# Kernel optimization log

Hardware: AMD Instinct MI355X
Metric: run time of the kernel (lower is better)

The kernel has to match this reference:

```python
import jax, jax.numpy as jnp
import numpy as np

D_MODEL = 1024
NHEADS = 16
DIM_K = D_MODEL // NHEADS


def setup_inputs() -> dict:
    key = jax.random.key(0)
    ks = jax.random.split(key, 7)
    B, S = 4, 2048
    scale = 1.0 / np.sqrt(D_MODEL)
    return {
        "Q": jax.random.normal(ks[0], (B, S, D_MODEL), jnp.float32),
        "K": jax.random.normal(ks[1], (B, S, D_MODEL), jnp.float32),
        "V": jax.random.normal(ks[2], (B, S, D_MODEL), jnp.float32),
        "Wq": jax.random.normal(ks[3], (D_MODEL, D_MODEL), jnp.float32) * scale,
        "Wk": jax.random.normal(ks[4], (D_MODEL, D_MODEL), jnp.float32) * scale,
        "Wv": jax.random.normal(ks[5], (D_MODEL, D_MODEL), jnp.float32) * scale,
        "Wo": jax.random.normal(ks[6], (D_MODEL, D_MODEL), jnp.float32) * scale,
    }


def _split(x):
    # [B,S,D] -> [B,H,S,dk]
    B, S, _ = x.shape
    return x.reshape(B, S, NHEADS, DIM_K).transpose(0, 2, 1, 3)


def reference(Q, K, V, Wq, Wk, Wv, Wo):
    # nn.Linear(x) = x @ W.T; weights stored torch-style [out, in]
    q = _split(Q @ Wq.T)  # [B,H,S,dk]
    k = _split(K @ Wk.T)
    v = _split(V @ Wv.T)
    scores = jnp.einsum("bhsd,bhtd->bhst", q, k) / jnp.sqrt(jnp.float32(DIM_K))
    attn = jax.nn.softmax(scores, axis=-1)
    out = jnp.einsum("bhst,bhtd->bhsd", attn, v)  # [B,H,S,dk]
    B, H, S, dk = out.shape
    out = out.transpose(0, 2, 1, 3).reshape(B, S, H * dk)
    return out @ Wo.T
```

## Files before the change

kernel.cpp:

```cpp
#include <hip/hip_runtime.h>
#include <math.h>
#include <stdint.h>

#define D_MODEL 1024
#define NHEADS  16
#define DK      64
#define BATCH   4
#define SEQ     2048
#define MROWS   (BATCH * SEQ)
#define TENS    ((size_t)MROWS * D_MODEL)
#define WELT    ((size_t)D_MODEL * D_MODEL)

typedef __attribute__((ext_vector_type(8))) _Float16 f16x8;
typedef __attribute__((ext_vector_type(2))) __fp16 h16x2;
typedef __attribute__((ext_vector_type(4))) float f32x4;
typedef __attribute__((ext_vector_type(8))) unsigned short us8;
typedef __attribute__((ext_vector_type(4))) unsigned short us4;

__device__ __forceinline__ unsigned short f2h(float x) {
    _Float16 h = (_Float16)x;
    return __builtin_bit_cast(unsigned short, h);
}

#if __has_builtin(__builtin_amdgcn_exp2f)
__device__ __forceinline__ float fexp2(float x) { return __builtin_amdgcn_exp2f(x); }
#else
__device__ __forceinline__ float fexp2(float x) { return exp2f(x); }
#endif

__device__ __forceinline__ void gld_lds16(const void* g, void* l) {
    __builtin_amdgcn_global_load_lds(
        (__attribute__((address_space(1))) void*)(uintptr_t)(g),
        (__attribute__((address_space(3))) void*)(unsigned)(uintptr_t)(l),
        16, 0, 0);
}

__global__ __launch_bounds__(256)
void convert_kernel(const float* __restrict__ q, const float* __restrict__ k,
                    const float* __restrict__ v, const float* __restrict__ wq,
                    const float* __restrict__ wk, const float* __restrict__ wv,
                    const float* __restrict__ wo, unsigned short* __restrict__ dst)
{
    const int seg = blockIdx.y;
    size_t i = ((size_t)blockIdx.x * 256 + threadIdx.x) * 4;
    const float* src;
    size_t doff, soff;
    if (seg < 3) {
        if (i >= TENS) return;
        src = (seg == 0) ? q : (seg == 1) ? k : v;
        soff = i;
        doff = (size_t)seg * TENS + i;
    } else {
        if (i >= 4 * WELT) return;
        const int widx = (int)(i >> 20);
        src = (widx == 0) ? wq : (widx == 1) ? wk : (widx == 2) ? wv : wo;
        soff = i & (WELT - 1);
        doff = 3 * TENS + i;
    }
    float4 f = *(const float4*)(src + soff);
    us4 o = { f2h(f.x), f2h(f.y), f2h(f.z), f2h(f.w) };
    *(us4*)(dst + doff) = o;
}

__device__ __forceinline__
void gemm_body8(const unsigned short* __restrict__ A,
                const unsigned short* __restrict__ B,
                void* __restrict__ C, int N, int K, int omode,
                unsigned short* As, unsigned short* Bs)
{
    const int tid  = threadIdx.x;
    const int wave = tid >> 6;
    const int lane = tid & 63;
    const int g    = lane >> 4;
    const int m15  = lane & 15;
    const int bm   = blockIdx.x * 256;
    const int bn   = blockIdx.y * 128;

    const int srw = lane >> 3;
    const int lc  = (lane & 7) ^ srw;

    const int wr = (wave >> 1) * 64;
    const int wc = (wave & 1) * 64;

    f32x4 acc[4][4];
#pragma unroll
    for (int i = 0; i < 4; ++i)
#pragma unroll
        for (int j = 0; j < 4; ++j) acc[i][j] = (f32x4){0.f, 0.f, 0.f, 0.f};

    auto stage = [&](int buf, int t) {
        const int k0 = t * 64;
#pragma unroll
        for (int i = 0; i < 4; ++i) {
            const int rb = i * 64 + wave * 8;
            gld_lds16(A + (size_t)(bm + rb + srw) * K + k0 + lc * 8,
                      &As[buf * (256 * 64) + rb * 64]);
        }
#pragma unroll
        for (int j = 0; j < 2; ++j) {
            const int rb = j * 64 + wave * 8;
            gld_lds16(B + (size_t)(bn + rb + srw) * K + k0 + lc * 8,
                      &Bs[buf * (128 * 64) + rb * 64]);
        }
    };

    auto compute = [&](int buf) {
        const unsigned short* Ab = &As[buf * (256 * 64)];
        const unsigned short* Bb = &Bs[buf * (128 * 64)];
#pragma unroll
        for (int t = 0; t < 2; ++t) {
            f16x8 af[4], bf[4];
#pragma unroll
            for (int i = 0; i < 4; ++i) {
                int row = wr + i * 16 + m15;
                int pc  = (4 * t + g) ^ (row & 7);
                af[i] = *(const f16x8*)&Ab[row * 64 + pc * 8];
            }
#pragma unroll
            for (int j = 0; j < 4; ++j) {
                int row = wc + j * 16 + m15;
                int pc  = (4 * t + g) ^ (row & 7);
                bf[j] = *(const f16x8*)&Bb[row * 64 + pc * 8];
            }
            __builtin_amdgcn_s_setprio(1);
#pragma unroll
            for (int i = 0; i < 4; ++i)
#pragma unroll
                for (int j = 0; j < 4; ++j)
                    acc[i][j] = __builtin_amdgcn_mfma_f32_16x16x32_f16(
                        af[i], bf[j], acc[i][j], 0, 0, 0);
            __builtin_amdgcn_s_setprio(0);
        }
    };

    const int NT = K / 64;
    stage(0, 0);
    stage(1, 1);
    int cur = 0;
    for (int t = 0; t < NT; ++t) {
        if (t + 2 < NT) {
            int nb = cur + 2; if (nb >= 3) nb -= 3;
            stage(nb, t + 2);
            asm volatile("s_waitcnt vmcnt(12)" ::: "memory");
        } else if (t + 1 < NT) {
            asm volatile("s_waitcnt vmcnt(6)" ::: "memory");
        } else {
            asm volatile("s_waitcnt vmcnt(0)" ::: "memory");
        }
        __builtin_amdgcn_s_barrier();
        __builtin_amdgcn_sched_barrier(0);
        compute(cur);
        __builtin_amdgcn_sched_barrier(0);
        __builtin_amdgcn_s_barrier();
        ++cur; if (cur == 3) cur = 0;
    }

#pragma unroll
    for (int i = 0; i < 4; ++i) {
        const int gm0 = bm + wr + i * 16 + g * 4;
#pragma unroll
        for (int j = 0; j < 4; ++j) {
            const int gn = bn + wc + j * 16 + m15;
            if (omode == 0) {
#pragma unroll
                for (int r = 0; r < 4; ++r)
                    ((float*)C)[(size_t)(gm0 + r) * N + gn] = acc[i][j][r];
            } else if (omode == 1) {
#pragma unroll
                for (int r = 0; r < 4; ++r)
                    ((unsigned short*)C)[(size_t)(gm0 + r) * N + gn] = f2h(acc[i][j][r]);
            } else {
                const int b_ = gm0 >> 11, s_ = gm0 & 2047;
                const int h_ = gn >> 6,  d_ = gn & 63;
                us4 o = { f2h(acc[i][j][0]), f2h(acc[i][j][1]),
                          f2h(acc[i][j][2]), f2h(acc[i][j][3]) };
                *(us4*)((unsigned short*)C +
                        (((size_t)(b_ * NHEADS + h_) * 256 + (s_ >> 3)) * 64 + d_) * 8
                        + (s_ & 7)) = o;
            }
        }
    }
}

__global__ __launch_bounds__(512)
void proj3_kernel(const unsigned short* __restrict__ qb,
                  const unsigned short* __restrict__ kb,
                  const unsigned short* __restrict__ vb,
                  const unsigned short* __restrict__ wq,
                  const unsigned short* __restrict__ wk,
                  const unsigned short* __restrict__ wv,
                  unsigned short* __restrict__ qproj,
                  unsigned short* __restrict__ kproj,
                  unsigned short* __restrict__ vtw)
{
    __shared__ unsigned short As[3 * 256 * 64];
    __shared__ unsigned short Bs[3 * 128 * 64];
    const int z = blockIdx.z;
    const unsigned short* A = (z == 0) ? qb : (z == 1) ? kb : vb;
    const unsigned short* B = (z == 0) ? wq : (z == 1) ? wk : wv;
    void* C = (z == 0) ? (void*)qproj : (z == 1) ? (void*)kproj : (void*)vtw;
    gemm_body8(A, B, C, D_MODEL, D_MODEL, (z == 2) ? 2 : 1, As, Bs);
}

__global__ __launch_bounds__(512)
void gemm_out_kernel(const unsigned short* __restrict__ A,
                     const unsigned short* __restrict__ B,
                     float* __restrict__ C)
{
    __shared__ unsigned short As[3 * 256 * 64];
    __shared__ unsigned short Bs[3 * 128 * 64];
    gemm_body8(A, B, C, D_MODEL, D_MODEL, 0, As, Bs);
}

__global__ __launch_bounds__(256, 2)
void attn_kernel(const unsigned short* __restrict__ qp,
                 const unsigned short* __restrict__ kp,
                 const unsigned short* __restrict__ vt,
                 unsigned short* __restrict__ ao)
{
    __shared__ unsigned short Ks[2][64 * 64];
    __shared__ unsigned short VTs[2][64 * 64];
    __shared__ unsigned short Ps[4][16 * 72];

    const int tid = threadIdx.x;
    const int w = tid >> 6, lane = tid & 63;
    const int g = lane >> 4, m15 = lane & 15;
    const int qt = blockIdx.x, h = blockIdx.y, b = blockIdx.z;

    const int q0 = qt * 256 + w * 64;
    const size_t rowbase = (size_t)b * SEQ;

    const int srw = lane >> 3;
    const int lc  = (lane & 7) ^ srw;

    const _Float16 qscale = (_Float16)(0.125f * 1.4426950408889634f);
    f16x8 qf[4][2];
#pragma unroll
    for (int mi = 0; mi < 4; ++mi)
#pragma unroll
        for (int t = 0; t < 2; ++t) {
            f16x8 v = *(const f16x8*)(qp + (rowbase + q0 + mi * 16 + m15) * D_MODEL
                                      + h * DK + t * 32 + g * 8);
            qf[mi][t] = v * qscale;
        }

    const _Float16 one16 = (_Float16)1.f;
    const f16x8 onesf = { one16, one16, one16, one16, one16, one16, one16, one16 };

    float mrun[4] = {-INFINITY, -INFINITY, -INFINITY, -INFINITY};
    float lrun[4] = {0.f, 0.f, 0.f, 0.f};

    f32x4 accO[4][4];
#pragma unroll
    for (int mi = 0; mi < 4; ++mi)
#pragma unroll
        for (int i = 0; i < 4; ++i) accO[mi][i] = (f32x4){0.f, 0.f, 0.f, 0.f};

    const unsigned short* kbase = kp + rowbase * D_MODEL + h * DK;
    const unsigned short* vbase = vt + (size_t)(b * NHEADS + h) * DK * SEQ;

    auto stage = [&](int buf, int t) {
#pragma unroll
        for (int it = 0; it < 2; ++it) {
            const int rb = w * 16 + it * 8;
            gld_lds16(kbase + (size_t)(t * 64 + rb + srw) * D_MODEL + lc * 8,
                      &Ks[buf][rb * 64]);
            gld_lds16(vbase + ((size_t)(t * 8 + lc) * 64 + rb + srw) * 8,
                      &VTs[buf][rb * 64]);
        }
    };

    const int NT = SEQ / 64;
    stage(0, 0);
    __syncthreads();

    for (int kt = 0; kt < NT; ++kt) {
        const int cur = kt & 1;
        if (kt + 1 < NT) stage(cur ^ 1, kt + 1);

        f32x4 ST[4][4];
        __builtin_amdgcn_s_setprio(1);
#pragma unroll
        for (int km = 0; km < 4; ++km) {
            const int row = km * 16 + m15;
            f16x8 kf0 = *(const f16x8*)&Ks[cur][row * 64 + ((0 + g) ^ (row & 7)) * 8];
            f16x8 kf1 = *(const f16x8*)&Ks[cur][row * 64 + ((4 + g) ^ (row & 7)) * 8];
#pragma unroll
            for (int mi = 0; mi < 4; ++mi) {
                f32x4 z = (f32x4){0.f, 0.f, 0.f, 0.f};
                z = __builtin_amdgcn_mfma_f32_16x16x32_f16(kf0, qf[mi][0], z, 0, 0, 0);
                z = __builtin_amdgcn_mfma_f32_16x16x32_f16(kf1, qf[mi][1], z, 0, 0, 0);
                ST[km][mi] = z;
            }
        }
        __builtin_amdgcn_s_setprio(0);

        float scl[4];
        f16x8 pf[4][2];
#pragma unroll
        for (int mi = 0; mi < 4; ++mi) {
            float t0 = fmaxf(fmaxf(ST[0][mi][0], ST[0][mi][1]), ST[0][mi][2]);
            float t1 = fmaxf(fmaxf(ST[0][mi][3], ST[1][mi][0]), ST[1][mi][1]);
            float t2 = fmaxf(fmaxf(ST[1][mi][2], ST[1][mi][3]), ST[2][mi][0]);
            float t3 = fmaxf(fmaxf(ST[2][mi][1], ST[2][mi][2]), ST[2][mi][3]);
            float t4 = fmaxf(fmaxf(ST[3][mi][0], ST[3][mi][1]), ST[3][mi][2]);
            float u0 = fmaxf(fmaxf(t0, t1), t2);
            float u1 = fmaxf(fmaxf(t3, t4), ST[3][mi][3]);
            float mx = fmaxf(u0, u1);
            mx = fmaxf(mx, __shfl_xor(mx, 16));
            mx = fmaxf(mx, __shfl_xor(mx, 32));
            float mnew = fmaxf(mrun[mi], mx);
            scl[mi] = fexp2(mrun[mi] - mnew);
            mrun[mi] = mnew;
#pragma unroll
            for (int km = 0; km < 4; ++km) {
                float p0 = fexp2(ST[km][mi][0] - mnew);
                float p1 = fexp2(ST[km][mi][1] - mnew);
                float p2 = fexp2(ST[km][mi][2] - mnew);
                float p3 = fexp2(ST[km][mi][3] - mnew);
                h16x2 d0 = __builtin_amdgcn_cvt_pkrtz(p0, p1);
                h16x2 d1 = __builtin_amdgcn_cvt_pkrtz(p2, p3);
                uint2 wv = { __builtin_bit_cast(unsigned, d0),
                             __builtin_bit_cast(unsigned, d1) };
                *(uint2*)&Ps[w][m15 * 72 + km * 16 + g * 4] = wv;
            }
            pf[mi][0] = *(const f16x8*)&Ps[w][m15 * 72 + g * 8];
            pf[mi][1] = *(const f16x8*)&Ps[w][m15 * 72 + 32 + g * 8];
            f32x4 zs = (f32x4){0.f, 0.f, 0.f, 0.f};
            zs = __builtin_amdgcn_mfma_f32_16x16x32_f16(onesf, pf[mi][0], zs, 0, 0, 0);
            zs = __builtin_amdgcn_mfma_f32_16x16x32_f16(onesf, pf[mi][1], zs, 0, 0, 0);
            lrun[mi] = lrun[mi] * scl[mi] + zs[0];
        }

        int chg = (scl[0] < 1.f) | (scl[1] < 1.f) | (scl[2] < 1.f) | (scl[3] < 1.f);
        if (__any(chg)) {
#pragma unroll
            for (int mi = 0; mi < 4; ++mi)
#pragma unroll
                for (int i = 0; i < 4; ++i) accO[mi][i] *= scl[mi];
        }

        __builtin_amdgcn_s_setprio(1);
#pragma unroll
        for (int i = 0; i < 4; ++i) {
            const int row = i * 16 + m15;
            f16x8 vf0 = *(const f16x8*)&VTs[cur][row * 64 + ((0 + g) ^ (row & 7)) * 8];
            f16x8 vf1 = *(const f16x8*)&VTs[cur][row * 64 + ((4 + g) ^ (row & 7)) * 8];
#pragma unroll
            for (int mi = 0; mi < 4; ++mi) {
                f32x4 a = accO[mi][i];
                a = __builtin_amdgcn_mfma_f32_16x16x32_f16(vf0, pf[mi][0], a, 0, 0, 0);
                a = __builtin_amdgcn_mfma_f32_16x16x32_f16(vf1, pf[mi][1], a, 0, 0, 0);
                accO[mi][i] = a;
            }
        }
        __builtin_amdgcn_s_setprio(0);

        __syncthreads();
    }

#pragma unroll
    for (int mi = 0; mi < 4; ++mi) {
        const float li = 1.f / lrun[mi];
        const size_t qg = rowbase + q0 + mi * 16 + m15;
#pragma unroll
        for (int i = 0; i < 4; ++i) {
            us4 o = { f2h(accO[mi][i][0] * li), f2h(accO[mi][i][1] * li),
                      f2h(accO[mi][i][2] * li), f2h(accO[mi][i][3] * li) };
            *(us4*)(ao + qg * D_MODEL + h * DK + i * 16 + g * 4) = o;
        }
    }
}

extern "C" void kernel_launch(void* const* d_in, const int* in_sizes, int n_in,
                              void* d_out, int out_size, void* d_ws, size_t ws_size,
                              hipStream_t stream)
{
    const float* Q  = (const float*)d_in[0];
    const float* K  = (const float*)d_in[1];
    const float* V  = (const float*)d_in[2];
    const float* Wq = (const float*)d_in[3];
    const float* Wk = (const float*)d_in[4];
    const float* Wv = (const float*)d_in[5];
    const float* Wo = (const float*)d_in[6];

    unsigned short* base = (unsigned short*)d_ws;
    unsigned short* qb = base;
    unsigned short* kb = qb + TENS;
    unsigned short* vb = kb + TENS;
    unsigned short* wq = vb + TENS;
    unsigned short* wk = wq + WELT;
    unsigned short* wv = wk + WELT;
    unsigned short* wo = wv + WELT;
    unsigned short* qproj = wo + WELT;
    unsigned short* kproj = qproj + TENS;
    unsigned short* vtw   = kproj + TENS;
    unsigned short* aow   = vtw + TENS;

    convert_kernel<<<dim3(TENS / 1024, 4), 256, 0, stream>>>(Q, K, V, Wq, Wk, Wv, Wo, base);

    proj3_kernel<<<dim3(MROWS / 256, D_MODEL / 128, 3), 512, 0, stream>>>(
        qb, kb, vb, wq, wk, wv, qproj, kproj, vtw);

    attn_kernel<<<dim3(SEQ / 256, NHEADS, BATCH), 256, 0, stream>>>(
        qproj, kproj, vtw, aow);

    gemm_out_kernel<<<dim3(MROWS / 256, D_MODEL / 128), 512, 0, stream>>>(
        aow, wo, (float*)d_out);
}
```

Baseline: 329.6 us.

## Shrink GEMM tiles to 128x128 with double buffering; keep attention P in registers

The projection and output GEMMs move from 256x128 tiles with 512 threads and triple-buffered LDS to 128x128 tiles with 256 threads, two LDS buffers and two blocks per CU. The next tile is now staged after the compute barrier. In attention, the softmax probabilities no longer round-trip through LDS. The code switches to 16x16x16 MFMAs whose B-operand layout matches the score accumulator registers, so P can feed the PV and row-sum MFMAs directly. This trades LDS traffic and a per-wave scratch buffer for twice as many MFMA issues, plus a shallower prefetch pipeline in the GEMMs.

New measurement: 343.3 us. 1.04x slower.

```diff
diff --git a/kernel.cpp b/kernel.cpp
--- a/kernel.cpp
+++ b/kernel.cpp
@@ -12,6 +12,7 @@
 #define WELT    ((size_t)D_MODEL * D_MODEL)
 
 typedef __attribute__((ext_vector_type(8))) _Float16 f16x8;
+typedef __attribute__((ext_vector_type(4))) _Float16 f16x4;
 typedef __attribute__((ext_vector_type(2))) __fp16 h16x2;
 typedef __attribute__((ext_vector_type(4))) float f32x4;
 typedef __attribute__((ext_vector_type(8))) unsigned short us8;
@@ -27,6 +28,15 @@
 #else
 __device__ __forceinline__ float fexp2(float x) { return exp2f(x); }
 #endif
+
+__device__ __forceinline__ f32x4 mfma16(f16x4 a, f16x4 b, f32x4 c) {
+#if __has_builtin(__builtin_amdgcn_mfma_f32_16x16x16f16)
+    return __builtin_amdgcn_mfma_f32_16x16x16f16(a, b, c, 0, 0, 0);
+#else
+    asm("v_mfma_f32_16x16x16_f16 %0, %1, %2, %0" : "+v"(c) : "v"(a), "v"(b));
+    return c;
+#endif
+}
 
 __device__ __forceinline__ void gld_lds16(const void* g, void* l) {
     __builtin_amdgcn_global_load_lds(
@@ -63,17 +73,17 @@
 }
 
 __device__ __forceinline__
-void gemm_body8(const unsigned short* __restrict__ A,
-                const unsigned short* __restrict__ B,
-                void* __restrict__ C, int N, int K, int omode,
-                unsigned short* As, unsigned short* Bs)
+void gemm_body(const unsigned short* __restrict__ A,
+               const unsigned short* __restrict__ B,
+               void* __restrict__ C, int N, int K, int omode,
+               unsigned short* As, unsigned short* Bs)
 {
     const int tid  = threadIdx.x;
     const int wave = tid >> 6;
     const int lane = tid & 63;
     const int g    = lane >> 4;
     const int m15  = lane & 15;
-    const int bm   = blockIdx.x * 256;
+    const int bm   = blockIdx.x * 128;
     const int bn   = blockIdx.y * 128;
 
     const int srw = lane >> 3;
@@ -92,20 +102,16 @@
         const int k0 = t * 64;
 #pragma unroll
         for (int i = 0; i < 4; ++i) {
-            const int rb = i * 64 + wave * 8;
+            const int rb = wave * 32 + i * 8;
             gld_lds16(A + (size_t)(bm + rb + srw) * K + k0 + lc * 8,
-                      &As[buf * (256 * 64) + rb * 64]);
-        }
-#pragma unroll
-        for (int j = 0; j < 2; ++j) {
-            const int rb = j * 64 + wave * 8;
+                      &As[buf * (128 * 64) + rb * 64]);
             gld_lds16(B + (size_t)(bn + rb + srw) * K + k0 + lc * 8,
                       &Bs[buf * (128 * 64) + rb * 64]);
         }
     };
 
     auto compute = [&](int buf) {
-        const unsigned short* Ab = &As[buf * (256 * 64)];
+        const unsigned short* Ab = &As[buf * (128 * 64)];
         const unsigned short* Bb = &Bs[buf * (128 * 64)];
 #pragma unroll
         for (int t = 0; t < 2; ++t) {
@@ -138,12 +144,8 @@
     stage(1, 1);
     int cur = 0;
     for (int t = 0; t < NT; ++t) {
-        if (t + 2 < NT) {
-            int nb = cur + 2; if (nb >= 3) nb -= 3;
-            stage(nb, t + 2);
-            asm volatile("s_waitcnt vmcnt(12)" ::: "memory");
-        } else if (t + 1 < NT) {
-            asm volatile("s_waitcnt vmcnt(6)" ::: "memory");
+        if (t + 1 < NT) {
+            asm volatile("s_waitcnt vmcnt(8)" ::: "memory");
         } else {
             asm volatile("s_waitcnt vmcnt(0)" ::: "memory");
         }
@@ -152,7 +154,8 @@
         compute(cur);
         __builtin_amdgcn_sched_barrier(0);
         __builtin_amdgcn_s_barrier();
-        ++cur; if (cur == 3) cur = 0;
+        if (t + 2 < NT) stage(cur, t + 2);
+        cur ^= 1;
     }
 
 #pragma unroll
@@ -182,7 +185,7 @@
     }
 }
 
-__global__ __launch_bounds__(512)
+__global__ __launch_bounds__(256, 2)
 void proj3_kernel(const unsigned short* __restrict__ qb,
                   const unsigned short* __restrict__ kb,
                   const unsigned short* __restrict__ vb,
@@ -193,23 +196,23 @@
                   unsigned short* __restrict__ kproj,
                   unsigned short* __restrict__ vtw)
 {
-    __shared__ unsigned short As[3 * 256 * 64];
-    __shared__ unsigned short Bs[3 * 128 * 64];
+    __shared__ unsigned short As[2 * 128 * 64];
+    __shared__ unsigned short Bs[2 * 128 * 64];
     const int z = blockIdx.z;
     const unsigned short* A = (z == 0) ? qb : (z == 1) ? kb : vb;
     const unsigned short* B = (z == 0) ? wq : (z == 1) ? wk : wv;
     void* C = (z == 0) ? (void*)qproj : (z == 1) ? (void*)kproj : (void*)vtw;
-    gemm_body8(A, B, C, D_MODEL, D_MODEL, (z == 2) ? 2 : 1, As, Bs);
-}
-
-__global__ __launch_bounds__(512)
+    gemm_body(A, B, C, D_MODEL, D_MODEL, (z == 2) ? 2 : 1, As, Bs);
+}
+
+__global__ __launch_bounds__(256, 2)
 void gemm_out_kernel(const unsigned short* __restrict__ A,
                      const unsigned short* __restrict__ B,
                      float* __restrict__ C)
 {
-    __shared__ unsigned short As[3 * 256 * 64];
-    __shared__ unsigned short Bs[3 * 128 * 64];
-    gemm_body8(A, B, C, D_MODEL, D_MODEL, 0, As, Bs);
+    __shared__ unsigned short As[2 * 128 * 64];
+    __shared__ unsigned short Bs[2 * 128 * 64];
+    gemm_body(A, B, C, D_MODEL, D_MODEL, 0, As, Bs);
 }
 
 __global__ __launch_bounds__(256, 2)
@@ -220,7 +223,6 @@
 {
     __shared__ unsigned short Ks[2][64 * 64];
     __shared__ unsigned short VTs[2][64 * 64];
-    __shared__ unsigned short Ps[4][16 * 72];
 
     const int tid = threadIdx.x;
     const int w = tid >> 6, lane = tid & 63;
@@ -245,7 +247,7 @@
         }
 
     const _Float16 one16 = (_Float16)1.f;
-    const f16x8 onesf = { one16, one16, one16, one16, one16, one16, one16, one16 };
+    const f16x4 ones4 = { one16, one16, one16, one16 };
 
     float mrun[4] = {-INFINITY, -INFINITY, -INFINITY, -INFINITY};
     float lrun[4] = {0.f, 0.f, 0.f, 0.f};
@@ -296,7 +298,7 @@
         __builtin_amdgcn_s_setprio(0);
 
         float scl[4];
-        f16x8 pf[4][2];
+        f16x4 pb[4][4];
 #pragma unroll
         for (int mi = 0; mi < 4; ++mi) {
             float t0 = fmaxf(fmaxf(ST[0][mi][0], ST[0][mi][1]), ST[0][mi][2]);
@@ -322,13 +324,11 @@
                 h16x2 d1 = __builtin_amdgcn_cvt_pkrtz(p2, p3);
                 uint2 wv = { __builtin_bit_cast(unsigned, d0),
                              __builtin_bit_cast(unsigned, d1) };
-                *(uint2*)&Ps[w][m15 * 72 + km * 16 + g * 4] = wv;
-            }
-            pf[mi][0] = *(const f16x8*)&Ps[w][m15 * 72 + g * 8];
-            pf[mi][1] = *(const f16x8*)&Ps[w][m15 * 72 + 32 + g * 8];
+                pb[mi][km] = __builtin_bit_cast(f16x4, wv);
+            }
             f32x4 zs = (f32x4){0.f, 0.f, 0.f, 0.f};
-            zs = __builtin_amdgcn_mfma_f32_16x16x32_f16(onesf, pf[mi][0], zs, 0, 0, 0);
-            zs = __builtin_amdgcn_mfma_f32_16x16x32_f16(onesf, pf[mi][1], zs, 0, 0, 0);
+#pragma unroll
+            for (int km = 0; km < 4; ++km) zs = mfma16(ones4, pb[mi][km], zs);
             lrun[mi] = lrun[mi] * scl[mi] + zs[0];
         }
 
@@ -344,13 +344,17 @@
 #pragma unroll
         for (int i = 0; i < 4; ++i) {
             const int row = i * 16 + m15;
-            f16x8 vf0 = *(const f16x8*)&VTs[cur][row * 64 + ((0 + g) ^ (row & 7)) * 8];
-            f16x8 vf1 = *(const f16x8*)&VTs[cur][row * 64 + ((4 + g) ^ (row & 7)) * 8];
+            f16x4 vf[4];
+#pragma unroll
+            for (int km = 0; km < 4; ++km) {
+                const int pc = (km * 2 + (g >> 1)) ^ (row & 7);
+                vf[km] = *(const f16x4*)&VTs[cur][row * 64 + pc * 8 + (g & 1) * 4];
+            }
 #pragma unroll
             for (int mi = 0; mi < 4; ++mi) {
                 f32x4 a = accO[mi][i];
-                a = __builtin_amdgcn_mfma_f32_16x16x32_f16(vf0, pf[mi][0], a, 0, 0, 0);
-                a = __builtin_amdgcn_mfma_f32_16x16x32_f16(vf1, pf[mi][1], a, 0, 0, 0);
+#pragma unroll
+                for (int km = 0; km < 4; ++km) a = mfma16(vf[km], pb[mi][km], a);
                 accO[mi][i] = a;
             }
         }
@@ -399,12 +403,12 @@
 
     convert_kernel<<<dim3(TENS / 1024, 4), 256, 0, stream>>>(Q, K, V, Wq, Wk, Wv, Wo, base);
 
-    proj3_kernel<<<dim3(MROWS / 256, D_MODEL / 128, 3), 512, 0, stream>>>(
+    proj3_kernel<<<dim3(MROWS / 128, D_MODEL / 128, 3), 256, 0, stream>>>(
         qb, kb, vb, wq, wk, wv, qproj, kproj, vtw);
 
     attn_kernel<<<dim3(SEQ / 256, NHEADS, BATCH), 256, 0, stream>>>(
         qproj, kproj, vtw, aow);
 
-    gemm_out_kernel<<<dim3(MROWS / 256, D_MODEL / 128), 512, 0, stream>>>(
+    gemm_out_kernel<<<dim3(MROWS / 128, D_MODEL / 128), 256, 0, stream>>>(
         aow, wo, (float*)d_out);
 }
```

## Remap block order for L2 locality and use lazy softmax rescaling

Applied to the files above, without the earlier changes.

Grids for the projection, attention and output GEMM kernels are flattened to 1D and decoded so that consecutive blocks spread across the 8 XCDs while each XCD handles contiguous panels or heads, which should improve L2 reuse. The attention softmax now rescales the running max only when a tile's local max exceeds the stored max by a threshold of 8 in the log2 domain, skipping cross-lane shuffles and exp on most iterations. P is staged in a swizzled 64-wide LDS layout instead of padded 72-wide rows. Lazy rescaling lets exponentials reach up to 2^8 before normalisation, which risks precision loss in fp16 P.

New measurement: 320.6 us. 1.03x faster.

```diff
diff --git a/kernel.cpp b/kernel.cpp
--- a/kernel.cpp
+++ b/kernel.cpp
@@ -66,6 +66,7 @@
 void gemm_body8(const unsigned short* __restrict__ A,
                 const unsigned short* __restrict__ B,
                 void* __restrict__ C, int N, int K, int omode,
+                int bm, int bn,
                 unsigned short* As, unsigned short* Bs)
 {
     const int tid  = threadIdx.x;
@@ -73,8 +74,6 @@
     const int lane = tid & 63;
     const int g    = lane >> 4;
     const int m15  = lane & 15;
-    const int bm   = blockIdx.x * 256;
-    const int bn   = blockIdx.y * 128;
 
     const int srw = lane >> 3;
     const int lc  = (lane & 7) ^ srw;
@@ -182,6 +181,15 @@
     }
 }
 
+__device__ __forceinline__ void panel_decode(int f, int& bm, int& bn) {
+    const int x = f & 7;
+    const int k = f >> 3;
+    const int panel = x * 4 + (k >> 3);
+    const int ny = k & 7;
+    bm = panel * 256;
+    bn = ny * 128;
+}
+
 __global__ __launch_bounds__(512)
 void proj3_kernel(const unsigned short* __restrict__ qb,
                   const unsigned short* __restrict__ kb,
@@ -199,7 +207,9 @@
     const unsigned short* A = (z == 0) ? qb : (z == 1) ? kb : vb;
     const unsigned short* B = (z == 0) ? wq : (z == 1) ? wk : wv;
     void* C = (z == 0) ? (void*)qproj : (z == 1) ? (void*)kproj : (void*)vtw;
-    gemm_body8(A, B, C, D_MODEL, D_MODEL, (z == 2) ? 2 : 1, As, Bs);
+    int bm, bn;
+    panel_decode(blockIdx.x, bm, bn);
+    gemm_body8(A, B, C, D_MODEL, D_MODEL, (z == 2) ? 2 : 1, bm, bn, As, Bs);
 }
 
 __global__ __launch_bounds__(512)
@@ -209,7 +219,9 @@
 {
     __shared__ unsigned short As[3 * 256 * 64];
     __shared__ unsigned short Bs[3 * 128 * 64];
-    gemm_body8(A, B, C, D_MODEL, D_MODEL, 0, As, Bs);
+    int bm, bn;
+    panel_decode(blockIdx.x, bm, bn);
+    gemm_body8(A, B, C, D_MODEL, D_MODEL, 0, bm, bn, As, Bs);
 }
 
 __global__ __launch_bounds__(256, 2)
@@ -220,12 +232,16 @@
 {
     __shared__ unsigned short Ks[2][64 * 64];
     __shared__ unsigned short VTs[2][64 * 64];
-    __shared__ unsigned short Ps[4][16 * 72];
+    __shared__ unsigned short Ps[4][16 * 64];
 
     const int tid = threadIdx.x;
     const int w = tid >> 6, lane = tid & 63;
     const int g = lane >> 4, m15 = lane & 15;
-    const int qt = blockIdx.x, h = blockIdx.y, b = blockIdx.z;
+
+    const int f = blockIdx.x;
+    const int bh = (f & 7) * 8 + ((f >> 3) >> 3);
+    const int qt = (f >> 3) & 7;
+    const int b = bh >> 4, h = bh & 15;
 
     const int q0 = qt * 256 + w * 64;
     const size_t rowbase = (size_t)b * SEQ;
@@ -295,8 +311,7 @@
         }
         __builtin_amdgcn_s_setprio(0);
 
-        float scl[4];
-        f16x8 pf[4][2];
+        float lmx[4];
 #pragma unroll
         for (int mi = 0; mi < 4; ++mi) {
             float t0 = fmaxf(fmaxf(ST[0][mi][0], ST[0][mi][1]), ST[0][mi][2]);
@@ -306,12 +321,30 @@
             float t4 = fmaxf(fmaxf(ST[3][mi][0], ST[3][mi][1]), ST[3][mi][2]);
             float u0 = fmaxf(fmaxf(t0, t1), t2);
             float u1 = fmaxf(fmaxf(t3, t4), ST[3][mi][3]);
-            float mx = fmaxf(u0, u1);
-            mx = fmaxf(mx, __shfl_xor(mx, 16));
-            mx = fmaxf(mx, __shfl_xor(mx, 32));
-            float mnew = fmaxf(mrun[mi], mx);
-            scl[mi] = fexp2(mrun[mi] - mnew);
-            mrun[mi] = mnew;
+            lmx[mi] = fmaxf(u0, u1);
+        }
+
+        const float THR = 8.f;
+        int need = (lmx[0] > mrun[0] + THR) | (lmx[1] > mrun[1] + THR) |
+                   (lmx[2] > mrun[2] + THR) | (lmx[3] > mrun[3] + THR);
+        if (__any(need)) {
+#pragma unroll
+            for (int mi = 0; mi < 4; ++mi) {
+                float mx = fmaxf(lmx[mi], __shfl_xor(lmx[mi], 16));
+                mx = fmaxf(mx, __shfl_xor(mx, 32));
+                float mnew = fmaxf(mrun[mi], mx);
+                float scl = fexp2(mrun[mi] - mnew);
+                mrun[mi] = mnew;
+                lrun[mi] *= scl;
+#pragma unroll
+                for (int i = 0; i < 4; ++i) accO[mi][i] *= scl;
+            }
+        }
+
+        f16x8 pf[4][2];
+#pragma unroll
+        for (int mi = 0; mi < 4; ++mi) {
+            const float mnew = mrun[mi];
 #pragma unroll
             for (int km = 0; km < 4; ++km) {
                 float p0 = fexp2(ST[km][mi][0] - mnew);
@@ -322,22 +355,15 @@
                 h16x2 d1 = __builtin_amdgcn_cvt_pkrtz(p2, p3);
                 uint2 wv = { __builtin_bit_cast(unsigned, d0),
                              __builtin_bit_cast(unsigned, d1) };
-                *(uint2*)&Ps[w][m15 * 72 + km * 16 + g * 4] = wv;
-            }
-            pf[mi][0] = *(const f16x8*)&Ps[w][m15 * 72 + g * 8];
-            pf[mi][1] = *(const f16x8*)&Ps[w][m15 * 72 + 32 + g * 8];
+                const int pc = (km * 2 + (g >> 1)) ^ (m15 & 7);
+                *(uint2*)&Ps[w][m15 * 64 + pc * 8 + (g & 1) * 4] = wv;
+            }
+            pf[mi][0] = *(const f16x8*)&Ps[w][m15 * 64 + ((0 + g) ^ (m15 & 7)) * 8];
+            pf[mi][1] = *(const f16x8*)&Ps[w][m15 * 64 + ((4 + g) ^ (m15 & 7)) * 8];
             f32x4 zs = (f32x4){0.f, 0.f, 0.f, 0.f};
             zs = __builtin_amdgcn_mfma_f32_16x16x32_f16(onesf, pf[mi][0], zs, 0, 0, 0);
             zs = __builtin_amdgcn_mfma_f32_16x16x32_f16(onesf, pf[mi][1], zs, 0, 0, 0);
-            lrun[mi] = lrun[mi] * scl[mi] + zs[0];
-        }
-
-        int chg = (scl[0] < 1.f) | (scl[1] < 1.f) | (scl[2] < 1.f) | (scl[3] < 1.f);
-        if (__any(chg)) {
-#pragma unroll
-            for (int mi = 0; mi < 4; ++mi)
-#pragma unroll
-                for (int i = 0; i < 4; ++i) accO[mi][i] *= scl[mi];
+            lrun[mi] += zs[0];
         }
 
         __builtin_amdgcn_s_setprio(1);
@@ -399,12 +425,12 @@
 
     convert_kernel<<<dim3(TENS / 1024, 4), 256, 0, stream>>>(Q, K, V, Wq, Wk, Wv, Wo, base);
 
-    proj3_kernel<<<dim3(MROWS / 256, D_MODEL / 128, 3), 512, 0, stream>>>(
+    proj3_kernel<<<dim3(256, 1, 3), 512, 0, stream>>>(
         qb, kb, vb, wq, wk, wv, qproj, kproj, vtw);
 
-    attn_kernel<<<dim3(SEQ / 256, NHEADS, BATCH), 256, 0, stream>>>(
+    attn_kernel<<<dim3(512, 1, 1), 256, 0, stream>>>(
         qproj, kproj, vtw, aow);
 
-    gemm_out_kernel<<<dim3(MROWS / 256, D_MODEL / 128), 512, 0, stream>>>(
+    gemm_out_kernel<<<dim3(256, 1, 1), 512, 0, stream>>>(
         aow, wo, (float*)d_out);
 }
```
